# Optimization experiments

Measured on AMD Instinct MI355X. Metric: run time of the kernel, lower is better.

Reference implementation:

```python
import jax, jax.numpy as jnp
import numpy as np

B, S, DIM, H = 2, 2048, 1024, 16
DH = DIM // H
ROPE_BASE = 10000.0
LOGIT_SCALE_INIT = 2.302585
EPS = 1e-6


def _rotate_half(x):
    # interleaved pairs: out[..., ::2] = -x[..., 1::2]; out[..., 1::2] = x[..., ::2]
    xr = x.reshape(x.shape[:-1] + (x.shape[-1] // 2, 2))
    out = jnp.stack([-xr[..., 1], xr[..., 0]], axis=-1)
    return out.reshape(x.shape)


def _rope_cos_sin(seq_len, head_dim, dtype):
    t = jnp.arange(seq_len, dtype=dtype)
    freqs = 1.0 / ROPE_BASE ** (jnp.arange(0, head_dim, 2, dtype=dtype) / head_dim)
    ang = t[:, None] * freqs[None, :]                # [S, Dh/2]
    emb = jnp.repeat(ang, 2, axis=-1)                # [S, Dh]
    return jnp.cos(emb)[None, None], jnp.sin(emb)[None, None]  # [1,1,S,Dh]


def _l2norm_last(x):
    return x / jnp.sqrt(jnp.sum(x * x, axis=-1, keepdims=True) + EPS)


def setup_inputs() -> dict:
    key = jax.random.key(0)
    ks = jax.random.split(key, 10)
    x = jax.random.normal(ks[0], (B, S, DIM), dtype=jnp.float32)
    # causal mask: True = masked (above diagonal)
    mask = jnp.broadcast_to(jnp.triu(jnp.ones((S, S), dtype=bool), k=1), (B, S, S))
    w = lambda k: jax.random.normal(k, (DIM, DIM), dtype=jnp.float32) * 0.02
    b = lambda k: jax.random.normal(k, (DIM,), dtype=jnp.float32) * 0.01
    return {
        "x": x,
        "Wq": w(ks[1]), "bq": b(ks[2]),
        "Wk": w(ks[3]), "bk": b(ks[4]),
        "Wv": w(ks[5]), "bv": b(ks[6]),
        "Wo": w(ks[7]), "bo": b(ks[8]),
        "logit_scale": jnp.float32(LOGIT_SCALE_INIT),
        "mask": mask,
    }


def reference(x, Wq, bq, Wk, bk, Wv, bv, Wo, bo, logit_scale, mask):
    Bx, Sx, Dm = x.shape
    Dh = Dm // H
    scale = Dh ** -0.5
    # projections (torch Linear: x @ W.T + b), split heads -> [B,H,S,Dh]
    q = (x @ Wq.T + bq).reshape(Bx, Sx, H, Dh).transpose(0, 2, 1, 3)
    k = (x @ Wk.T + bk).reshape(Bx, Sx, H, Dh).transpose(0, 2, 1, 3)
    v = (x @ Wv.T + bv).reshape(Bx, Sx, H, Dh).transpose(0, 2, 1, 3)
    cos, sin = _rope_cos_sin(Sx, Dh, x.dtype)
    q = q * cos + _rotate_half(q) * sin
    k = k * cos + _rotate_half(k) * sin
    q = _l2norm_last(q)
    k = _l2norm_last(k)
    scores = jnp.einsum('bhsd,bhtd->bhst', q, k) * scale * jnp.exp(logit_scale)
    scores = jnp.where(mask[:, None, :, :], -jnp.inf, scores)
    a = jax.nn.softmax(scores, axis=-1)
    out = jnp.einsum('bhst,bhtd->bhsd', a, v).transpose(0, 2, 1, 3).reshape(Bx, Sx, Dm)
    return out @ Wo.T + bo
```

## Files before the change

kernel.cpp:

```cpp
#include <hip/hip_runtime.h>
#include <hip/hip_bf16.h>
#include <math.h>

typedef __hip_bfloat16 bf16;
typedef __attribute__((ext_vector_type(8))) short short8;
typedef __attribute__((ext_vector_type(4))) float floatx4;

static constexpr int Bn = 2, Sn = 2048, Hn = 16, DHn = 64, DIMn = 1024;
static constexpr int Mn = Bn * Sn;

#if __has_builtin(__builtin_amdgcn_exp2f)
#define EXP2(x) __builtin_amdgcn_exp2f(x)
#else
#define EXP2(x) exp2f(x)
#endif

__device__ __forceinline__ unsigned short bfbits(float f) {
  union { __hip_bfloat16 h; unsigned short u; } cv;
  cv.h = __float2bfloat16(f);
  return cv.u;
}

__device__ __forceinline__ float bf2f(unsigned short u) {
  union { float f; unsigned int u; } cv;
  cv.u = ((unsigned int)u) << 16;
  return cv.f;
}

__device__ __forceinline__ unsigned int pack_bf16(float lo, float hi) {
  union { float f; unsigned int u; } a, b;
  a.f = lo; b.f = hi;
  return (b.u & 0xFFFF0000u) | (a.u >> 16);
}

__device__ __forceinline__ void gload_lds16(const void* g, void* l) {
  __builtin_amdgcn_global_load_lds(
      (const __attribute__((address_space(1))) uint32_t*)g,
      (__attribute__((address_space(3))) uint32_t*)l, 16, 0, 0);
}

template <int N>
__device__ __forceinline__ void wait_vm() {
  if constexpr (N == 0) asm volatile("s_waitcnt vmcnt(0)" ::: "memory");
  else if constexpr (N == 2) asm volatile("s_waitcnt vmcnt(2)" ::: "memory");
  else if constexpr (N == 3) asm volatile("s_waitcnt vmcnt(3)" ::: "memory");
  else if constexpr (N == 4) asm volatile("s_waitcnt vmcnt(4)" ::: "memory");
  else asm volatile("s_waitcnt vmcnt(6)" ::: "memory");
  __builtin_amdgcn_sched_barrier(0);
}

__global__ void prep_kernel(const float* __restrict__ x,
                            const float* __restrict__ a0, const float* __restrict__ a1,
                            const float* __restrict__ a2, const float* __restrict__ a3,
                            unsigned short* __restrict__ xo,
                            unsigned short* __restrict__ o0, unsigned short* __restrict__ o1,
                            unsigned short* __restrict__ o2, unsigned short* __restrict__ o3,
                            float* __restrict__ tc, float* __restrict__ ts) {
  const int bid = blockIdx.x;
  if (bid < 8192) {
    const float* s;
    unsigned short* d;
    int i;
    if (bid < 4096) {
      s = x; d = xo; i = bid * 256 + threadIdx.x;
    } else {
      int wsel = (bid - 4096) >> 10;
      s = (wsel == 0) ? a0 : (wsel == 1) ? a1 : (wsel == 2) ? a2 : a3;
      d = (wsel == 0) ? o0 : (wsel == 1) ? o1 : (wsel == 2) ? o2 : o3;
      i = ((bid - 4096) & 1023) * 256 + threadIdx.x;
    }
    float4 v = ((const float4*)s)[i];
    ushort4 o;
    o.x = bfbits(v.x); o.y = bfbits(v.y); o.z = bfbits(v.z); o.w = bfbits(v.w);
    ((ushort4*)d)[i] = o;
  } else {
    int t = (bid - 8192) * 256 + threadIdx.x;
    int pos = t >> 5, i = t & 31;
    float f = powf(10000.0f, -(float)i * (1.0f / 32.0f));
    float a = (float)pos * f;
    tc[t] = cosf(a);
    ts[t] = sinf(a);
  }
}

__global__ __launch_bounds__(256, 3) void qkv_kernel(
    const bf16* __restrict__ A,
    const bf16* __restrict__ Wq, const bf16* __restrict__ Wk, const bf16* __restrict__ Wv,
    const float* __restrict__ bq, const float* __restrict__ bk, const float* __restrict__ bv,
    const float* __restrict__ tc, const float* __restrict__ ts,
    unsigned short* __restrict__ qo, unsigned short* __restrict__ ko,
    unsigned short* __restrict__ vt) {
  __shared__ bf16 smem[24576];
  bf16* sAp = smem;
  bf16* sBp = smem + 16384;
  const int sel = blockIdx.y >> 4;
  const bf16* Bw = (sel == 0) ? Wq : (sel == 1) ? Wk : Wv;
  const float* bias = (sel == 0) ? bq : (sel == 1) ? bk : bv;
  const int tid = threadIdx.x;
  const int lane = tid & 63, wave = tid >> 6;
  const int fr = lane & 15, fq = lane >> 4;
  const int m0 = blockIdx.x * 128, n0 = (blockIdx.y & 15) * 64;

  floatx4 acc[2][4] = {};

  auto stage = [&](int buf, int k0) {
#pragma unroll
    for (int call = 0; call < 4; ++call) {
      int row = call * 32 + (tid >> 3);
      int sb = ((tid & 7) * 16) ^ ((row & 7) << 4);
      gload_lds16(A + (size_t)(m0 + row) * 1024 + k0 + sb / 2,
                  sAp + buf * 8192 + call * 2048 + wave * 512);
    }
#pragma unroll
    for (int call = 0; call < 2; ++call) {
      int row = call * 32 + (tid >> 3);
      int sb = ((tid & 7) * 16) ^ ((row & 7) << 4);
      gload_lds16(Bw + (size_t)(n0 + row) * 1024 + k0 + sb / 2,
                  sBp + buf * 4096 + call * 2048 + wave * 512);
    }
  };

  stage(0, 0);
  stage(1, 64);
  int cur = 0;
  for (int k0 = 0; k0 < 1024; k0 += 64) {
    if (k0 + 64 < 1024) wait_vm<6>(); else wait_vm<0>();
    __builtin_amdgcn_s_barrier();
    __builtin_amdgcn_sched_barrier(0);
    const char* sAc = (const char*)(sAp + cur * 8192);
    const char* sBc = (const char*)(sBp + cur * 4096);
    short8 af[2][2], bfr[4][2];
#pragma unroll
    for (int mi = 0; mi < 2; ++mi) {
      int arow = wave * 32 + mi * 16 + fr;
      int asw = (arow & 7) << 4;
#pragma unroll
      for (int kc = 0; kc < 2; ++kc)
        af[mi][kc] = *(const short8*)(sAc + arow * 128 + ((kc * 64 + fq * 16) ^ asw));
    }
#pragma unroll
    for (int ni = 0; ni < 4; ++ni) {
      int brow = ni * 16 + fr;
      int bsw = (brow & 7) << 4;
#pragma unroll
      for (int kc = 0; kc < 2; ++kc)
        bfr[ni][kc] = *(const short8*)(sBc + brow * 128 + ((kc * 64 + fq * 16) ^ bsw));
    }
#pragma unroll
    for (int mi = 0; mi < 2; ++mi)
#pragma unroll
      for (int ni = 0; ni < 4; ++ni)
#pragma unroll
        for (int kc = 0; kc < 2; ++kc)
          acc[mi][ni] = __builtin_amdgcn_mfma_f32_16x16x32_bf16(af[mi][kc], bfr[ni][kc],
                                                               acc[mi][ni], 0, 0, 0);
    __builtin_amdgcn_sched_barrier(0);
    __builtin_amdgcn_s_barrier();
    if (k0 + 128 < 1024) stage(cur, k0 + 128);
    cur ^= 1;
  }

  if (sel < 2) {
    unsigned short* dst = (sel == 0) ? qo : ko;
    const int h = n0 >> 6;
    float bias_d[4];
#pragma unroll
    for (int ni = 0; ni < 4; ++ni) bias_d[ni] = bias[n0 + ni * 16 + fr];
#pragma unroll
    for (int mi = 0; mi < 2; ++mi)
#pragma unroll
      for (int j = 0; j < 4; ++j) {
        int m = m0 + wave * 32 + mi * 16 + fq * 4 + j;
        int b = m >> 11, srow = m & 2047;
        float y[4], ss = 0.f;
#pragma unroll
        for (int ni = 0; ni < 4; ++ni) {
          float val = acc[mi][ni][j] + bias_d[ni];
          float prt = __shfl_xor(val, 1);
          int d = ni * 16 + fr;
          int jj = d >> 1;
          float cc = tc[srow * 32 + jj], sn = ts[srow * 32 + jj];
          y[ni] = (d & 1) ? (val * cc + prt * sn) : (val * cc - prt * sn);
          ss += y[ni] * y[ni];
        }
        ss += __shfl_xor(ss, 1);
        ss += __shfl_xor(ss, 2);
        ss += __shfl_xor(ss, 4);
        ss += __shfl_xor(ss, 8);
        float inv = rsqrtf(ss + 1e-6f);
        size_t ob = ((size_t)(b * 16 + h) * 2048 + srow) * 64;
#pragma unroll
        for (int ni = 0; ni < 4; ++ni)
          dst[ob + ni * 16 + fr] = bfbits(y[ni] * inv);
      }
  } else {
    __syncthreads();
    char* ct = (char*)smem;
#pragma unroll
    for (int mi = 0; mi < 2; ++mi)
#pragma unroll
      for (int ni = 0; ni < 4; ++ni) {
        int nl = ni * 16 + fr;
        float bi = bias[n0 + nl];
#pragma unroll
        for (int j = 0; j < 4; j += 2) {
          int ml = wave * 32 + mi * 16 + fq * 4 + j;
          unsigned int u = (unsigned int)bfbits(acc[mi][ni][j] + bi) |
                           ((unsigned int)bfbits(acc[mi][ni][j + 1] + bi) << 16);
          *(unsigned int*)(ct + nl * 256 + ((ml * 2) ^ ((nl & 15) << 4))) = u;
        }
      }
    __syncthreads();
    int nl2 = tid >> 2, ch = tid & 3;
    int h = n0 >> 6;
    int b = m0 >> 11, s0 = m0 & 2047;
    unsigned short* orow = vt + (((size_t)b * 16 + h) * 64 + nl2) * 2048 + s0;
    int swz = (nl2 & 15) << 4;
    int cb = 32 * (ch >> 1) + 16 * (ch & 1);
    const char* rowp = ct + nl2 * 256;
#pragma unroll
    for (int gix = 0; gix < 2; ++gix) {
      int gb = gix * 128;
      union { long long l[2]; short8 v; } s1, s2;
      s1.l[0] = *(const long long*)(rowp + ((gb + cb) ^ swz));
      s1.l[1] = *(const long long*)(rowp + ((gb + cb + 64) ^ swz));
      s2.l[0] = *(const long long*)(rowp + ((gb + cb + 8) ^ swz));
      s2.l[1] = *(const long long*)(rowp + ((gb + cb + 72) ^ swz));
      *(short8*)(orow + gix * 64 + ch * 16) = s1.v;
      *(short8*)(orow + gix * 64 + ch * 16 + 8) = s2.v;
    }
  }
}

__global__ __launch_bounds__(256, 3) void gemm_bt_kernel(
    const bf16* __restrict__ A, const bf16* __restrict__ Bw,
    const float* __restrict__ bias, float* __restrict__ Cf) {
  __shared__ bf16 smem[24576];
  bf16* sAp = smem;
  bf16* sBp = smem + 16384;
  const int tid = threadIdx.x;
  const int lane = tid & 63, wave = tid >> 6;
  const int fr = lane & 15, fq = lane >> 4;
  const int m0 = blockIdx.x * 128, n0 = blockIdx.y * 64;

  floatx4 acc[2][4] = {};

  auto stage = [&](int buf, int k0) {
#pragma unroll
    for (int call = 0; call < 4; ++call) {
      int row = call * 32 + (tid >> 3);
      int sb = ((tid & 7) * 16) ^ ((row & 7) << 4);
      gload_lds16(A + (size_t)(m0 + row) * 1024 + k0 + sb / 2,
                  sAp + buf * 8192 + call * 2048 + wave * 512);
    }
#pragma unroll
    for (int call = 0; call < 2; ++call) {
      int row = call * 32 + (tid >> 3);
      int sb = ((tid & 7) * 16) ^ ((row & 7) << 4);
      gload_lds16(Bw + (size_t)(n0 + row) * 1024 + k0 + sb / 2,
                  sBp + buf * 4096 + call * 2048 + wave * 512);
    }
  };

  stage(0, 0);
  stage(1, 64);
  int cur = 0;
  for (int k0 = 0; k0 < 1024; k0 += 64) {
    if (k0 + 64 < 1024) wait_vm<6>(); else wait_vm<0>();
    __builtin_amdgcn_s_barrier();
    __builtin_amdgcn_sched_barrier(0);
    const char* sAc = (const char*)(sAp + cur * 8192);
    const char* sBc = (const char*)(sBp + cur * 4096);
    short8 af[2][2], bfr[4][2];
#pragma unroll
    for (int mi = 0; mi < 2; ++mi) {
      int arow = wave * 32 + mi * 16 + fr;
      int asw = (arow & 7) << 4;
#pragma unroll
      for (int kc = 0; kc < 2; ++kc)
        af[mi][kc] = *(const short8*)(sAc + arow * 128 + ((kc * 64 + fq * 16) ^ asw));
    }
#pragma unroll
    for (int ni = 0; ni < 4; ++ni) {
      int brow = ni * 16 + fr;
      int bsw = (brow & 7) << 4;
#pragma unroll
      for (int kc = 0; kc < 2; ++kc)
        bfr[ni][kc] = *(const short8*)(sBc + brow * 128 + ((kc * 64 + fq * 16) ^ bsw));
    }
#pragma unroll
    for (int mi = 0; mi < 2; ++mi)
#pragma unroll
      for (int ni = 0; ni < 4; ++ni)
#pragma unroll
        for (int kc = 0; kc < 2; ++kc)
          acc[mi][ni] = __builtin_amdgcn_mfma_f32_16x16x32_bf16(af[mi][kc], bfr[ni][kc],
                                                               acc[mi][ni], 0, 0, 0);
    __builtin_amdgcn_sched_barrier(0);
    __builtin_amdgcn_s_barrier();
    if (k0 + 128 < 1024) stage(cur, k0 + 128);
    cur ^= 1;
  }

#pragma unroll
  for (int ni = 0; ni < 4; ++ni) {
    int n = n0 + ni * 16 + fr;
    float bi = bias[n];
#pragma unroll
    for (int mi = 0; mi < 2; ++mi)
#pragma unroll
      for (int j = 0; j < 4; ++j) {
        int m = m0 + wave * 32 + mi * 16 + fq * 4 + j;
        Cf[(size_t)m * 1024 + n] = acc[mi][ni][j] + bi;
      }
  }
}

__global__ __launch_bounds__(256, 5) void attn_kernel(
    const bf16* __restrict__ qb, const bf16* __restrict__ kb, const bf16* __restrict__ vt,
    const float* __restrict__ ls, unsigned short* __restrict__ out) {
  __shared__ bf16 sK[2][64 * 64];
  __shared__ bf16 sV[2][64 * 64];
  const int bid = blockIdx.x;
  const int rr4 = bid >> 8, g = bid & 255, jj = g & 31;
  const int xq = (rr4 & 1) ? (31 - jj) : jj;
  const int bh = (g >> 5) + 8 * rr4;
  const int q0A = xq * 32, q0B = (63 - xq) * 32;
  const int tid = threadIdx.x;
  const int lane = tid & 63, wave = tid >> 6;
  const int fr = lane & 15, fq = lane >> 4;
  const int myq0 = ((((wave >> 1) ^ bid) & 1)) ? q0B : q0A;
  const int base = myq0 + (wave & 1) * 16;
  float scl2 = __expf(ls[0]) * 0.125f * 1.44269504f;

  const size_t qrow = (size_t)bh * 2048 + base + fr;
  short8 qf0 = *(const short8*)(qb + qrow * 64 + fq * 8);
  short8 qf1 = *(const short8*)(qb + qrow * 64 + 32 + fq * 8);
  asm volatile("" : "+v"(qf0), "+v"(qf1), "+v"(scl2));
  __builtin_amdgcn_sched_barrier(0);

  const bf16* kgb = kb + (size_t)bh * 2048 * 64;
  const bf16* vgb = vt + (size_t)bh * 64 * 2048;

  auto stage = [&](int buf, int t0) {
#pragma unroll
    for (int call = 0; call < 2; ++call) {
      int row = call * 32 + (tid >> 3);
      int sb = ((tid & 7) * 16) ^ ((row & 7) << 4);
      gload_lds16(kgb + (size_t)(t0 + row) * 64 + sb / 2,
                  &sK[buf][call * 2048 + wave * 512]);
    }
#pragma unroll
    for (int call = 0; call < 2; ++call) {
      int row = call * 32 + (tid >> 3);
      int sb = ((tid & 7) * 16) ^ ((row & 7) << 4);
      gload_lds16(vgb + (size_t)row * 2048 + t0 + sb / 2,
                  &sV[buf][call * 2048 + wave * 512]);
    }
  };

  floatx4 oacc[4] = {};
  float m_l = -INFINITY, l_l = 0.f;
  const int qrow_l = base + fr;
  const int rowq = base + fq * 4;
  const int sw = (fr & 7) << 4;

  const int tEnd = q0B + 32;
  stage(0, 0);
  stage(1, 64);
  int cur = 0;
  for (int t0 = 0; t0 < tEnd; t0 += 64) {
    if (t0 + 64 < tEnd) wait_vm<4>(); else wait_vm<0>();
    __builtin_amdgcn_s_barrier();
    __builtin_amdgcn_sched_barrier(0);
    if (t0 < myq0 + 32) {
      const char* sKc = (const char*)sK[cur];
      const char* sVc = (const char*)sV[cur];
      floatx4 sacc[4] = {};
      __builtin_amdgcn_s_setprio(1);
#pragma unroll
      for (int c = 0; c < 4; ++c) {
        int rb = (c * 16 + fr) * 128;
        short8 kf0 = *(const short8*)(sKc + rb + ((fq * 16) ^ sw));
        short8 kf1 = *(const short8*)(sKc + rb + ((64 + fq * 16) ^ sw));
        sacc[c] = __builtin_amdgcn_mfma_f32_16x16x32_bf16(kf0, qf0, sacc[c], 0, 0, 0);
        sacc[c] = __builtin_amdgcn_mfma_f32_16x16x32_bf16(kf1, qf1, sacc[c], 0, 0, 0);
      }
      __builtin_amdgcn_s_setprio(0);
      if (t0 + 63 > base) {
#pragma unroll
        for (int c = 0; c < 4; ++c)
#pragma unroll
          for (int r = 0; r < 4; ++r)
            if ((t0 + c * 16 + fq * 4 + r) > qrow_l) sacc[c][r] = -1e30f;
      }
      float pm0 = fmaxf(fmaxf(sacc[0][0], sacc[0][1]), fmaxf(sacc[0][2], sacc[0][3]));
      float pm1 = fmaxf(fmaxf(sacc[1][0], sacc[1][1]), fmaxf(sacc[1][2], sacc[1][3]));
      float pm2 = fmaxf(fmaxf(sacc[2][0], sacc[2][1]), fmaxf(sacc[2][2], sacc[2][3]));
      float pm3 = fmaxf(fmaxf(sacc[3][0], sacc[3][1]), fmaxf(sacc[3][2], sacc[3][3]));
      float pm = fmaxf(fmaxf(pm0, pm1), fmaxf(pm2, pm3));
      if (!__all(pm * scl2 - m_l <= 11.5f)) {
        float pmr = fmaxf(pm, __shfl_xor(pm, 16));
        pmr = fmaxf(pmr, __shfl_xor(pmr, 32));
        float mnew = fmaxf(m_l, pmr * scl2);
        float rs = EXP2(m_l - mnew);
        m_l = mnew;
        l_l *= rs;
        float rsr[4];
#pragma unroll
        for (int r = 0; r < 4; ++r) rsr[r] = __shfl(rs, rowq - base + r);
#pragma unroll
        for (int d = 0; d < 4; ++d)
#pragma unroll
          for (int r = 0; r < 4; ++r) oacc[d][r] *= rsr[r];
      }
      float p[4][4];
      float ssum = 0.f;
#pragma unroll
      for (int c = 0; c < 4; ++c)
#pragma unroll
        for (int r = 0; r < 4; ++r) {
          p[c][r] = EXP2(sacc[c][r] * scl2 - m_l);
          ssum += p[c][r];
        }
      ssum += __shfl_xor(ssum, 16);
      ssum += __shfl_xor(ssum, 32);
      l_l += ssum;
      short8 pf[2];
#pragma unroll
      for (int kc = 0; kc < 2; ++kc) {
        union { unsigned int w[4]; short8 v; } pk;
        pk.w[0] = pack_bf16(p[kc][0], p[kc][1]);
        pk.w[1] = pack_bf16(p[kc][2], p[kc][3]);
        pk.w[2] = pack_bf16(p[kc + 2][0], p[kc + 2][1]);
        pk.w[3] = pack_bf16(p[kc + 2][2], p[kc + 2][3]);
        pf[kc] = pk.v;
      }
      __builtin_amdgcn_s_setprio(1);
#pragma unroll
      for (int d = 0; d < 4; ++d) {
        int rbv = (d * 16 + fr) * 128;
#pragma unroll
        for (int kc = 0; kc < 2; ++kc) {
          short8 vf = *(const short8*)(sVc + rbv + ((kc * 64 + fq * 16) ^ sw));
          oacc[d] = __builtin_amdgcn_mfma_f32_16x16x32_bf16(pf[kc], vf, oacc[d], 0, 0, 0);
        }
      }
      __builtin_amdgcn_s_setprio(0);
    }
    __builtin_amdgcn_sched_barrier(0);
    __builtin_amdgcn_s_barrier();
    if (t0 + 128 < tEnd) stage(cur, t0 + 128);
    cur ^= 1;
  }
  const int b = bh >> 4, h = bh & 15;
  float il[4];
#pragma unroll
  for (int r = 0; r < 4; ++r) il[r] = 1.0f / __shfl(l_l, rowq - base + r);
#pragma unroll
  for (int r = 0; r < 4; ++r)
#pragma unroll
    for (int d = 0; d < 4; ++d) {
      size_t o = ((size_t)b * 2048 + rowq + r) * 1024 + h * 64 + d * 16 + fr;
      out[o] = bfbits(oacc[d][r] * il[r]);
    }
}

extern "C" void kernel_launch(void* const* d_in, const int* in_sizes, int n_in,
                              void* d_out, int out_size, void* d_ws, size_t ws_size,
                              hipStream_t stream) {
  (void)in_sizes; (void)n_in; (void)out_size; (void)ws_size;
  const float* x  = (const float*)d_in[0];
  const float* Wq = (const float*)d_in[1];
  const float* bq = (const float*)d_in[2];
  const float* Wk = (const float*)d_in[3];
  const float* bk = (const float*)d_in[4];
  const float* Wv = (const float*)d_in[5];
  const float* bv = (const float*)d_in[6];
  const float* Wo = (const float*)d_in[7];
  const float* bo = (const float*)d_in[8];
  const float* lsc = (const float*)d_in[9];

  uint8_t* w = (uint8_t*)d_ws;
  const size_t MB = 1ull << 20;
  bf16* xb   = (bf16*)(w + 0);
  bf16* wqb  = (bf16*)(w + 8 * MB);
  bf16* wkb  = (bf16*)(w + 10 * MB);
  bf16* wvb  = (bf16*)(w + 12 * MB);
  bf16* wob  = (bf16*)(w + 14 * MB);
  bf16* qbn  = (bf16*)(w + 16 * MB);
  bf16* kbn  = (bf16*)(w + 24 * MB);
  bf16* vtb  = (bf16*)(w + 32 * MB);
  bf16* atb  = (bf16*)(w + 40 * MB);
  float* tc  = (float*)(w + 48 * MB);
  float* ts  = (float*)(w + 48 * MB + 256 * 1024);

  prep_kernel<<<8448, 256, 0, stream>>>(
      x, Wq, Wk, Wv, Wo, (unsigned short*)xb,
      (unsigned short*)wqb, (unsigned short*)wkb, (unsigned short*)wvb,
      (unsigned short*)wob, tc, ts);

  qkv_kernel<<<dim3(32, 48), 256, 0, stream>>>(
      xb, wqb, wkb, wvb, bq, bk, bv, tc, ts,
      (unsigned short*)qbn, (unsigned short*)kbn, (unsigned short*)vtb);

  attn_kernel<<<1024, 256, 0, stream>>>(qbn, kbn, vtb, lsc,
                                        (unsigned short*)atb);

  gemm_bt_kernel<<<dim3(32, 16), 256, 0, stream>>>(atb, wob, bo, (float*)d_out);
}
```

Measured before the change: 111.6 us.

## Widen QKV projection tile to 128x128 with single-buffered weight staging

The QKV GEMM block tile grows from 128x64 to 128x128, which halves the grid and doubles accumulator registers per thread. Each staged activation tile is now reused across twice as many output columns, and each block covers two heads in the RoPE/L2-norm and V-transpose epilogues. To stay within the same shared-memory budget, the weight tile is single-buffered and loaded only one k-step ahead. That exposes more of its load latency and raises register pressure, which may hurt occupancy.

```diff
diff --git a/kernel.cpp b/kernel.cpp
--- a/kernel.cpp
+++ b/kernel.cpp
@@ -93,17 +93,17 @@
   __shared__ bf16 smem[24576];
   bf16* sAp = smem;
   bf16* sBp = smem + 16384;
-  const int sel = blockIdx.y >> 4;
+  const int sel = blockIdx.y >> 3;
   const bf16* Bw = (sel == 0) ? Wq : (sel == 1) ? Wk : Wv;
   const float* bias = (sel == 0) ? bq : (sel == 1) ? bk : bv;
   const int tid = threadIdx.x;
   const int lane = tid & 63, wave = tid >> 6;
   const int fr = lane & 15, fq = lane >> 4;
-  const int m0 = blockIdx.x * 128, n0 = (blockIdx.y & 15) * 64;
-
-  floatx4 acc[2][4] = {};
-
-  auto stage = [&](int buf, int k0) {
+  const int m0 = blockIdx.x * 128, n0 = (blockIdx.y & 7) * 128;
+
+  floatx4 acc[2][8] = {};
+
+  auto stageA = [&](int buf, int k0) {
 #pragma unroll
     for (int call = 0; call < 4; ++call) {
       int row = call * 32 + (tid >> 3);
@@ -111,25 +111,28 @@
       gload_lds16(A + (size_t)(m0 + row) * 1024 + k0 + sb / 2,
                   sAp + buf * 8192 + call * 2048 + wave * 512);
     }
-#pragma unroll
-    for (int call = 0; call < 2; ++call) {
+  };
+  auto stageB = [&](int k0) {
+#pragma unroll
+    for (int call = 0; call < 4; ++call) {
       int row = call * 32 + (tid >> 3);
       int sb = ((tid & 7) * 16) ^ ((row & 7) << 4);
       gload_lds16(Bw + (size_t)(n0 + row) * 1024 + k0 + sb / 2,
-                  sBp + buf * 4096 + call * 2048 + wave * 512);
+                  sBp + call * 2048 + wave * 512);
     }
   };
 
-  stage(0, 0);
-  stage(1, 64);
+  stageB(0);
+  stageA(0, 0);
+  stageA(1, 64);
   int cur = 0;
   for (int k0 = 0; k0 < 1024; k0 += 64) {
-    if (k0 + 64 < 1024) wait_vm<6>(); else wait_vm<0>();
+    if (k0 + 64 < 1024) wait_vm<4>(); else wait_vm<0>();
     __builtin_amdgcn_s_barrier();
     __builtin_amdgcn_sched_barrier(0);
     const char* sAc = (const char*)(sAp + cur * 8192);
-    const char* sBc = (const char*)(sBp + cur * 4096);
-    short8 af[2][2], bfr[4][2];
+    const char* sBc = (const char*)sBp;
+    short8 af[2][2];
 #pragma unroll
     for (int mi = 0; mi < 2; ++mi) {
       int arow = wave * 32 + mi * 16 + fr;
@@ -139,59 +142,68 @@
         af[mi][kc] = *(const short8*)(sAc + arow * 128 + ((kc * 64 + fq * 16) ^ asw));
     }
 #pragma unroll
-    for (int ni = 0; ni < 4; ++ni) {
-      int brow = ni * 16 + fr;
-      int bsw = (brow & 7) << 4;
-#pragma unroll
-      for (int kc = 0; kc < 2; ++kc)
-        bfr[ni][kc] = *(const short8*)(sBc + brow * 128 + ((kc * 64 + fq * 16) ^ bsw));
-    }
-#pragma unroll
-    for (int mi = 0; mi < 2; ++mi)
-#pragma unroll
-      for (int ni = 0; ni < 4; ++ni)
+    for (int nh = 0; nh < 2; ++nh) {
+      short8 bfr[4][2];
+#pragma unroll
+      for (int n4 = 0; n4 < 4; ++n4) {
+        int brow = (nh * 4 + n4) * 16 + fr;
+        int bsw = (brow & 7) << 4;
 #pragma unroll
         for (int kc = 0; kc < 2; ++kc)
-          acc[mi][ni] = __builtin_amdgcn_mfma_f32_16x16x32_bf16(af[mi][kc], bfr[ni][kc],
-                                                               acc[mi][ni], 0, 0, 0);
+          bfr[n4][kc] = *(const short8*)(sBc + brow * 128 + ((kc * 64 + fq * 16) ^ bsw));
+      }
+#pragma unroll
+      for (int mi = 0; mi < 2; ++mi)
+#pragma unroll
+        for (int n4 = 0; n4 < 4; ++n4)
+#pragma unroll
+          for (int kc = 0; kc < 2; ++kc)
+            acc[mi][nh * 4 + n4] = __builtin_amdgcn_mfma_f32_16x16x32_bf16(
+                af[mi][kc], bfr[n4][kc], acc[mi][nh * 4 + n4], 0, 0, 0);
+    }
     __builtin_amdgcn_sched_barrier(0);
     __builtin_amdgcn_s_barrier();
-    if (k0 + 128 < 1024) stage(cur, k0 + 128);
+    if (k0 + 64 < 1024) stageB(k0 + 64);
+    if (k0 + 128 < 1024) stageA(cur, k0 + 128);
     cur ^= 1;
   }
 
   if (sel < 2) {
     unsigned short* dst = (sel == 0) ? qo : ko;
-    const int h = n0 >> 6;
-    float bias_d[4];
-#pragma unroll
-    for (int ni = 0; ni < 4; ++ni) bias_d[ni] = bias[n0 + ni * 16 + fr];
+    const int h0 = n0 >> 6;
+    float bias_d[8];
+#pragma unroll
+    for (int ni = 0; ni < 8; ++ni) bias_d[ni] = bias[n0 + ni * 16 + fr];
 #pragma unroll
     for (int mi = 0; mi < 2; ++mi)
 #pragma unroll
       for (int j = 0; j < 4; ++j) {
         int m = m0 + wave * 32 + mi * 16 + fq * 4 + j;
         int b = m >> 11, srow = m & 2047;
-        float y[4], ss = 0.f;
-#pragma unroll
-        for (int ni = 0; ni < 4; ++ni) {
-          float val = acc[mi][ni][j] + bias_d[ni];
-          float prt = __shfl_xor(val, 1);
-          int d = ni * 16 + fr;
-          int jj = d >> 1;
-          float cc = tc[srow * 32 + jj], sn = ts[srow * 32 + jj];
-          y[ni] = (d & 1) ? (val * cc + prt * sn) : (val * cc - prt * sn);
-          ss += y[ni] * y[ni];
+#pragma unroll
+        for (int hh = 0; hh < 2; ++hh) {
+          float y[4], ss = 0.f;
+#pragma unroll
+          for (int n4 = 0; n4 < 4; ++n4) {
+            int ni = hh * 4 + n4;
+            float val = acc[mi][ni][j] + bias_d[ni];
+            float prt = __shfl_xor(val, 1);
+            int d = n4 * 16 + fr;
+            int jj = d >> 1;
+            float cc = tc[srow * 32 + jj], sn = ts[srow * 32 + jj];
+            y[n4] = (d & 1) ? (val * cc + prt * sn) : (val * cc - prt * sn);
+            ss += y[n4] * y[n4];
+          }
+          ss += __shfl_xor(ss, 1);
+          ss += __shfl_xor(ss, 2);
+          ss += __shfl_xor(ss, 4);
+          ss += __shfl_xor(ss, 8);
+          float inv = rsqrtf(ss + 1e-6f);
+          size_t ob = ((size_t)(b * 16 + h0 + hh) * 2048 + srow) * 64;
+#pragma unroll
+          for (int n4 = 0; n4 < 4; ++n4)
+            dst[ob + n4 * 16 + fr] = bfbits(y[n4] * inv);
         }
-        ss += __shfl_xor(ss, 1);
-        ss += __shfl_xor(ss, 2);
-        ss += __shfl_xor(ss, 4);
-        ss += __shfl_xor(ss, 8);
-        float inv = rsqrtf(ss + 1e-6f);
-        size_t ob = ((size_t)(b * 16 + h) * 2048 + srow) * 64;
-#pragma unroll
-        for (int ni = 0; ni < 4; ++ni)
-          dst[ob + ni * 16 + fr] = bfbits(y[ni] * inv);
       }
   } else {
     __syncthreads();
@@ -199,7 +211,7 @@
 #pragma unroll
     for (int mi = 0; mi < 2; ++mi)
 #pragma unroll
-      for (int ni = 0; ni < 4; ++ni) {
+      for (int ni = 0; ni < 8; ++ni) {
         int nl = ni * 16 + fr;
         float bi = bias[n0 + nl];
 #pragma unroll
@@ -211,23 +223,23 @@
         }
       }
     __syncthreads();
-    int nl2 = tid >> 2, ch = tid & 3;
-    int h = n0 >> 6;
+    int nl2 = tid >> 1, half = tid & 1;
+    int head = (n0 >> 6) + (nl2 >> 6), dd = nl2 & 63;
     int b = m0 >> 11, s0 = m0 & 2047;
-    unsigned short* orow = vt + (((size_t)b * 16 + h) * 64 + nl2) * 2048 + s0;
+    unsigned short* orow =
+        vt + (((size_t)b * 16 + head) * 64 + dd) * 2048 + s0 + half * 64;
     int swz = (nl2 & 15) << 4;
-    int cb = 32 * (ch >> 1) + 16 * (ch & 1);
     const char* rowp = ct + nl2 * 256;
 #pragma unroll
-    for (int gix = 0; gix < 2; ++gix) {
-      int gb = gix * 128;
+    for (int ch = 0; ch < 4; ++ch) {
+      int cb = half * 128 + 32 * (ch >> 1) + 16 * (ch & 1);
       union { long long l[2]; short8 v; } s1, s2;
-      s1.l[0] = *(const long long*)(rowp + ((gb + cb) ^ swz));
-      s1.l[1] = *(const long long*)(rowp + ((gb + cb + 64) ^ swz));
-      s2.l[0] = *(const long long*)(rowp + ((gb + cb + 8) ^ swz));
-      s2.l[1] = *(const long long*)(rowp + ((gb + cb + 72) ^ swz));
-      *(short8*)(orow + gix * 64 + ch * 16) = s1.v;
-      *(short8*)(orow + gix * 64 + ch * 16 + 8) = s2.v;
+      s1.l[0] = *(const long long*)(rowp + ((cb) ^ swz));
+      s1.l[1] = *(const long long*)(rowp + ((cb + 64) ^ swz));
+      s2.l[0] = *(const long long*)(rowp + ((cb + 8) ^ swz));
+      s2.l[1] = *(const long long*)(rowp + ((cb + 72) ^ swz));
+      *(short8*)(orow + ch * 16) = s1.v;
+      *(short8*)(orow + ch * 16 + 8) = s2.v;
     }
   }
 }
@@ -500,7 +512,7 @@
       (unsigned short*)wqb, (unsigned short*)wkb, (unsigned short*)wvb,
       (unsigned short*)wob, tc, ts);
 
-  qkv_kernel<<<dim3(32, 48), 256, 0, stream>>>(
+  qkv_kernel<<<dim3(32, 24), 256, 0, stream>>>(
       xb, wqb, wkb, wvb, bq, bk, bv, tc, ts,
       (unsigned short*)qbn, (unsigned short*)kbn, (unsigned short*)vtb);
 
```

Result: faster. 108.1 us (median of 2 runs) (-3.1%).
